# Kernel optimization log

Hardware: AMD Instinct MI355X
Metric: run time of the kernel (lower is better)

## Reference

```python
import jax, jax.numpy as jnp
import numpy as np

N = 50000      # nodes
E = 500000     # edges
MUL = 32       # multiplicity of 0e and 1o in node irreps
NUM_NEIGHBORS = 10.0
MIX = 0.15
INV3 = 1.0 / np.sqrt(3.0)  # sqrt(2*l3+1)*wigner_3j(1,1,0) = delta_ij/sqrt(3)


def setup_inputs() -> dict:
    key = jax.random.key(0)
    ks = jax.random.split(key, 16)
    f32 = jnp.float32
    node_input = jax.random.normal(ks[0], (N, 128), dtype=f32)  # 32x0e (32) + 32x1o (96)
    # edge_attr = spherical harmonics lmax=1, component normalization: Y0=1, |Y1|=sqrt(3)
    y1 = jax.random.normal(ks[1], (E, 3), dtype=f32)
    y1 = jnp.sqrt(3.0) * y1 / jnp.linalg.norm(y1, axis=1, keepdims=True)
    edge_attr = jnp.concatenate([jnp.ones((E, 1), f32), y1], axis=1)  # [E,4]
    edge_scalars = jax.random.uniform(ks[2], (E, 8), dtype=f32)       # radial embedding
    edge_src = jax.random.randint(ks[3], (E,), 0, N)
    edge_dst = jax.random.randint(ks[4], (E,), 0, N)
    rn = lambda k, s: jax.random.normal(k, s, dtype=f32)
    return {
        "node_input": node_input, "edge_attr": edge_attr, "edge_scalars": edge_scalars,
        "W1_s": rn(ks[5], (MUL, 2 * MUL)),  # first Linear, 0e block: 32 -> 64 (=feat 32 + self 32)
        "W1_v": rn(ks[6], (MUL, 2 * MUL)),  # first Linear, 1o block
        "M0": rn(ks[7], (8, 32)), "M1": rn(ks[8], (32, 32)),  # weight MLP (fc_neurons=[32,32])
        "Wtp0": rn(ks[9], (32, MUL)),   # path 0e x 0e -> 0e
        "Wtp1": rn(ks[10], (32, MUL)),  # path 0e x 1o -> 1o
        "Wtp2": rn(ks[11], (32, MUL)),  # path 1o x 0e -> 1o
        "Wtp3": rn(ks[12], (32, MUL)),  # path 1o x 1o -> 0e
        "W2_s": rn(ks[13], (2 * MUL, MUL)),  # final Linear, 0e: 64 -> 32
        "W2_v": rn(ks[14], (2 * MUL, MUL)),  # final Linear, 1o: 64 -> 32
        "edge_src": edge_src, "edge_dst": edge_dst,
    }


def _forward(node_input, edge_attr, edge_scalars, W1_s, W1_v, M0, M1,
             Wtp0, Wtp1, Wtp2, Wtp3, W2_s, W2_v, edge_src, edge_dst):
    n = node_input.shape[0]
    s = node_input[:, :MUL]                       # [N,32]  0e
    v = node_input[:, MUL:].reshape(n, MUL, 3)    # [N,32,3] 1o
    # Linear(node_input.irreps + irreps_out): per-irrep mixing, fan-in normalized
    s_all = (s @ W1_s) / jnp.sqrt(jnp.float32(MUL))                    # [N,64]
    v_all = jnp.einsum('nuk,uw->nwk', v, W1_v) / jnp.sqrt(jnp.float32(MUL))  # [N,64,3]
    feat_s, self_s = s_all[:, :MUL], s_all[:, MUL:]
    feat_v, self_v = v_all[:, :MUL], v_all[:, MUL:]

    # gather by edge source
    es = feat_s[edge_src]   # [E,32]
    ev = feat_v[edge_src]   # [E,32,3]
    y0 = edge_attr[:, 0]    # [E]
    y1 = edge_attr[:, 1:4]  # [E,3]

    # MLP on edge scalars -> per-edge, per-path 'uvu' weights (fan-in normalized)
    h = jax.nn.gelu(edge_scalars @ M0 / jnp.sqrt(jnp.float32(8)))
    h = jax.nn.gelu(h @ M1 / jnp.sqrt(jnp.float32(32)))                # [E,32]
    inv_sqrt_h = 1.0 / jnp.sqrt(jnp.float32(32))
    w0 = (h @ Wtp0) * inv_sqrt_h  # [E,32]
    w1 = (h @ Wtp1) * inv_sqrt_h
    w2 = (h @ Wtp2) * inv_sqrt_h
    w3 = (h @ Wtp3) * inv_sqrt_h

    # per-edge CG tensor product (4 'uvu' instructions)
    out0a = w0 * es * y0[:, None]                                    # 0e x 0e -> 0e
    out0b = w3 * jnp.einsum('euk,ek->eu', ev, y1) * INV3             # 1o x 1o -> 0e
    out1a = w1[:, :, None] * es[:, :, None] * y1[:, None, :]        # 0e x 1o -> 1o
    out1b = w2[:, :, None] * ev * y0[:, None, None]                 # 1o x 0e -> 1o
    out0 = jnp.concatenate([out0a, out0b], axis=1)                  # [E,64]  64x0e
    out1 = jnp.concatenate([out1a, out1b], axis=1)                  # [E,64,3] 64x1o

    # scatter-add to destination nodes, normalize by sqrt(num_neighbors)
    inv_deg = 1.0 / jnp.sqrt(jnp.float32(NUM_NEIGHBORS))
    ns = jax.ops.segment_sum(out0, edge_dst, num_segments=n) * inv_deg              # [N,64]
    nv = jax.ops.segment_sum(out1.reshape(-1, 2 * MUL * 3), edge_dst,
                             num_segments=n).reshape(n, 2 * MUL, 3) * inv_deg       # [N,64,3]

    # final per-irrep Linear to output irreps 32x0e + 32x1o
    conv_s = (ns @ W2_s) / jnp.sqrt(jnp.float32(2 * MUL))
    conv_v = jnp.einsum('nuk,uw->nwk', nv, W2_v) / jnp.sqrt(jnp.float32(2 * MUL))

    a = jnp.sqrt(jnp.float32(1.0 - MIX))
    b = jnp.sqrt(jnp.float32(MIX))
    out_s = a * self_s + b * conv_s                                  # [N,32]
    out_v = (a * self_v + b * conv_v).reshape(n, MUL * 3)            # [N,96]
    return jnp.concatenate([out_s, out_v], axis=1)                   # [N,128]


def reference(node_input, edge_attr, edge_scalars, W1_s, W1_v, M0, M1,
              Wtp0, Wtp1, Wtp2, Wtp3, W2_s, W2_v, edge_src, edge_dst):
    return _forward(node_input, edge_attr, edge_scalars, W1_s, W1_v, M0, M1,
                    Wtp0, Wtp1, Wtp2, Wtp3, W2_s, W2_v, edge_src, edge_dst)
```

## Files before the change

### kernel.cpp

```cpp
#include <hip/hip_runtime.h>
#include <math.h>

#define N_NODES 50000
#define N_EDGES 500000
#define NPB 16
#define GROUPS 8

__device__ __forceinline__ float gelu_fast(float x) {
    const float k0 = 0.7978845608028654f;
    const float k1 = 0.044715f;
    float z2 = 2.f * k0 * (x + k1 * x * x * x);
    float ez = __expf(z2);
    float th = 1.f - 2.f * __builtin_amdgcn_rcpf(ez + 1.f);
    return 0.5f * x * (1.f + th);
}

__device__ __forceinline__ unsigned short f2bf(float x) {
    unsigned int u = __float_as_uint(x);
    unsigned int r = (u + 0x7FFFu + ((u >> 16) & 1u)) >> 16;
    return (unsigned short)r;
}
__device__ __forceinline__ float bf2f(unsigned short b) {
    return __uint_as_float(((unsigned int)b) << 16);
}

__device__ __forceinline__ void lds_add(float* p, float v) {
    unsigned int off = (unsigned int)(size_t)p;
    asm volatile("ds_add_f32 %0, %1" :: "v"(off), "v"(v) : "memory");
}

__global__ void node_pre(const float* __restrict__ node_input,
                         const float* __restrict__ W1_s,
                         const float* __restrict__ W1_v,
                         float* __restrict__ feat,
                         float* __restrict__ out) {
    __shared__ float lWs[32 * 64];
    __shared__ float lWv[32 * 64];
    for (int i = threadIdx.x; i < 2048; i += blockDim.x) {
        lWs[i] = W1_s[i];
        lWv[i] = W1_v[i];
    }
    __syncthreads();
    int n = blockIdx.x * blockDim.x + threadIdx.x;
    if (n >= N_NODES) return;
    const float inv_sqrt_mul = 0.17677669529663687f;
    const float a_mix = 0.9219544457292887f;

    float s[32];
#pragma unroll
    for (int u = 0; u < 32; ++u) s[u] = node_input[n * 128 + u];
#pragma unroll 4
    for (int w = 0; w < 64; ++w) {
        float acc = 0.f;
#pragma unroll
        for (int u = 0; u < 32; ++u) acc += s[u] * lWs[u * 64 + w];
        acc *= inv_sqrt_mul;
        if (w < 32) feat[(size_t)n * 128 + w * 4 + 0] = acc;
        else        out[n * 128 + (w - 32)] = a_mix * acc;
    }
#pragma unroll
    for (int k = 0; k < 3; ++k) {
        float vk[32];
#pragma unroll
        for (int u = 0; u < 32; ++u) vk[u] = node_input[n * 128 + 32 + u * 3 + k];
#pragma unroll 4
        for (int w = 0; w < 64; ++w) {
            float acc = 0.f;
#pragma unroll
            for (int u = 0; u < 32; ++u) acc += vk[u] * lWv[u * 64 + w];
            acc *= inv_sqrt_mul;
            if (w < 32) feat[(size_t)n * 128 + w * 4 + 1 + k] = acc;
            else        out[n * 128 + 32 + (w - 32) * 3 + k] = a_mix * acc;
        }
    }
}

__global__ void hist_kernel(const int* __restrict__ edge_dst, int* __restrict__ counts) {
    int e = blockIdx.x * blockDim.x + threadIdx.x;
    if (e < N_EDGES) atomicAdd(&counts[edge_dst[e]], 1);
}

__global__ void scan_kernel(const int* __restrict__ counts,
                            int* __restrict__ offsets,
                            int* __restrict__ cursor) {
    const int T = 1024;
    __shared__ int partial[T];
    int t = threadIdx.x;
    const int chunk = (N_NODES + T - 1) / T;
    int start = t * chunk;
    int end = start + chunk; if (end > N_NODES) end = N_NODES;
    if (start > N_NODES) start = N_NODES;
    int sum = 0;
    for (int i = start; i < end; ++i) sum += counts[i];
    partial[t] = sum;
    __syncthreads();
    for (int off = 1; off < T; off <<= 1) {
        int other = (t >= off) ? partial[t - off] : 0;
        __syncthreads();
        partial[t] += other;
        __syncthreads();
    }
    int run = (t == 0) ? 0 : partial[t - 1];
    for (int i = start; i < end; ++i) {
        offsets[i] = run;
        cursor[i] = run;
        run += counts[i];
    }
    if (t == T - 1) offsets[N_NODES] = run;
}

__global__ void scatter_kernel(const int* __restrict__ edge_src,
                               const int* __restrict__ edge_dst,
                               const float* __restrict__ edge_attr,
                               const float* __restrict__ edge_scalars,
                               int* __restrict__ cursor,
                               float4* __restrict__ sS4,
                               float4* __restrict__ ySorted,
                               int2* __restrict__ srcdst) {
    int e = blockIdx.x * blockDim.x + threadIdx.x;
    if (e >= N_EDGES) return;
    int d = edge_dst[e];
    int pos = atomicAdd(&cursor[d], 1);
    float4 a  = *(const float4*)(edge_attr + (size_t)e * 4);
    float4 s0 = *(const float4*)(edge_scalars + (size_t)e * 8);
    float4 s1 = *(const float4*)(edge_scalars + (size_t)e * 8 + 4);
    ySorted[pos] = a;
    sS4[(size_t)pos * 2 + 0] = s0;
    sS4[(size_t)pos * 2 + 1] = s1;
    srcdst[pos] = make_int2(edge_src[e], d);
}

__global__ void mlp_kernel(const float4* __restrict__ sS4,
                           const float* __restrict__ M0,
                           const float* __restrict__ M1,
                           const float* __restrict__ Wtp0,
                           const float* __restrict__ Wtp1,
                           const float* __restrict__ Wtp2,
                           const float* __restrict__ Wtp3,
                           ushort4* __restrict__ wOut) {
    const int e = blockIdx.x * blockDim.x + threadIdx.x;
    if (e >= N_EDGES) return;

    const float inv_sqrt8  = 0.35355339059327373f;
    const float inv_sqrt32 = 0.17677669529663687f;

    const float4 s0 = sS4[(size_t)e * 2 + 0];
    const float4 s1 = sS4[(size_t)e * 2 + 1];

    float t[32];
#pragma unroll
    for (int u = 0; u < 32; ++u) {
        float acc = s0.x * M0[0 * 32 + u] + s0.y * M0[1 * 32 + u]
                  + s0.z * M0[2 * 32 + u] + s0.w * M0[3 * 32 + u]
                  + s1.x * M0[4 * 32 + u] + s1.y * M0[5 * 32 + u]
                  + s1.z * M0[6 * 32 + u] + s1.w * M0[7 * 32 + u];
        t[u] = gelu_fast(acc * inv_sqrt8);
    }
    float h[32];
#pragma unroll
    for (int u = 0; u < 32; ++u) {
        float acc = 0.f;
#pragma unroll
        for (int m = 0; m < 32; ++m) acc += t[m] * M1[m * 32 + u];
        h[u] = gelu_fast(acc * inv_sqrt32);
    }
    ushort4* wbase = wOut + (size_t)e * 32;
#pragma unroll 1
    for (int u = 0; u < 32; ++u) {
        float ax = 0.f, ay = 0.f, az = 0.f, aw = 0.f;
#pragma unroll
        for (int j = 0; j < 32; ++j) {
            const float hj = h[j];
            ax += hj * Wtp0[j * 32 + u];
            ay += hj * Wtp1[j * 32 + u];
            az += hj * Wtp2[j * 32 + u];
            aw += hj * Wtp3[j * 32 + u];
        }
        ushort4 o;
        o.x = f2bf(ax * inv_sqrt32);
        o.y = f2bf(ay * inv_sqrt32);
        o.z = f2bf(az * inv_sqrt32);
        o.w = f2bf(aw * inv_sqrt32);
        wbase[u] = o;
    }
}

__global__ void __launch_bounds__(256)
conv_kernel(const ushort4* __restrict__ wOut,
            const float4* __restrict__ ySorted,
            const int2* __restrict__ srcdst,
            const int* __restrict__ offsets,
            const float* __restrict__ W2_s,
            const float* __restrict__ W2_v,
            const float* __restrict__ feat,
            float* __restrict__ out) {
    __shared__ float sacc[NPB * 256];
    for (int i = threadIdx.x; i < NPB * 256; i += blockDim.x) sacc[i] = 0.f;
    __syncthreads();

    const int lane = threadIdx.x & 31;
    const int g = threadIdx.x >> 5;
    const int n0 = blockIdx.x * NPB;
    const int eb = offsets[n0];
    const int ee = offsets[n0 + NPB];
    const float INV3 = 0.5773502691896258f;
    const float4* feat4 = (const float4*)feat;

    const int total = ee - eb;
    const int per = (total + GROUPS - 1) / GROUPS;
    const int es = eb + g * per;
    int et = es + per; if (et > ee) et = ee;

    float r0 = 0.f, r1 = 0.f, r2 = 0.f, r3 = 0.f;
    float r4 = 0.f, r5 = 0.f, r6 = 0.f, r7 = 0.f;
    int cur = -1;

#pragma unroll 2
    for (int e = es; e < et; ++e) {
        const int2 sd = srcdst[e];
        const ushort4 wq = wOut[(size_t)e * 32 + lane];
        const float4 yq = ySorted[e];
        const float4 f = feat4[(size_t)sd.x * 32 + lane];

        if (sd.y != cur) {
            if (cur >= 0) {
                float* a = sacc + (cur - n0) * 256;
                lds_add(a + lane, r0);
                lds_add(a + 32 + lane, r1);
                lds_add(a + 64 + lane * 3 + 0, r2);
                lds_add(a + 64 + lane * 3 + 1, r3);
                lds_add(a + 64 + lane * 3 + 2, r4);
                lds_add(a + 160 + lane * 3 + 0, r5);
                lds_add(a + 160 + lane * 3 + 1, r6);
                lds_add(a + 160 + lane * 3 + 2, r7);
            }
            cur = sd.y;
            r0 = r1 = r2 = r3 = r4 = r5 = r6 = r7 = 0.f;
        }

        const float w0 = bf2f(wq.x), w1 = bf2f(wq.y);
        const float w2 = bf2f(wq.z), w3 = bf2f(wq.w);
        const float dvy = f.y * yq.y + f.z * yq.z + f.w * yq.w;
        const float w1es = w1 * f.x;
        const float w2y0 = w2 * yq.x;

        r0 += w0 * f.x * yq.x;
        r1 += w3 * dvy * INV3;
        r2 += w1es * yq.y;
        r3 += w1es * yq.z;
        r4 += w1es * yq.w;
        r5 += w2y0 * f.y;
        r6 += w2y0 * f.z;
        r7 += w2y0 * f.w;
    }
    if (cur >= 0) {
        float* a = sacc + (cur - n0) * 256;
        lds_add(a + lane, r0);
        lds_add(a + 32 + lane, r1);
        lds_add(a + 64 + lane * 3 + 0, r2);
        lds_add(a + 64 + lane * 3 + 1, r3);
        lds_add(a + 64 + lane * 3 + 2, r4);
        lds_add(a + 160 + lane * 3 + 0, r5);
        lds_add(a + 160 + lane * 3 + 1, r6);
        lds_add(a + 160 + lane * 3 + 2, r7);
    }
    asm volatile("s_waitcnt lgkmcnt(0)" ::: "memory");
    __syncthreads();

    const float scale = 0.31622776601683794f * 0.125f * 0.3872983346207417f;
    for (int li = g; li < NPB; li += GROUPS) {
        const float* a = sacc + li * 256;
        float cs = 0.f, cv0 = 0.f, cv1 = 0.f, cv2 = 0.f;
#pragma unroll 8
        for (int j = 0; j < 64; ++j) {
            const float as = a[j];
            cs += as * __ldg(&W2_s[j * 32 + lane]);
            const float wv = __ldg(&W2_v[j * 32 + lane]);
            cv0 += a[64 + 3 * j + 0] * wv;
            cv1 += a[64 + 3 * j + 1] * wv;
            cv2 += a[64 + 3 * j + 2] * wv;
        }
        float* o = out + (size_t)(n0 + li) * 128;
        o[lane]              += scale * cs;
        o[32 + lane * 3 + 0] += scale * cv0;
        o[32 + lane * 3 + 1] += scale * cv1;
        o[32 + lane * 3 + 2] += scale * cv2;
    }
}

extern "C" void kernel_launch(void* const* d_in, const int* in_sizes, int n_in,
                              void* d_out, int out_size, void* d_ws, size_t ws_size,
                              hipStream_t stream) {
    const float* node_input   = (const float*)d_in[0];
    const float* edge_attr    = (const float*)d_in[1];
    const float* edge_scalars = (const float*)d_in[2];
    const float* W1_s = (const float*)d_in[3];
    const float* W1_v = (const float*)d_in[4];
    const float* M0   = (const float*)d_in[5];
    const float* M1   = (const float*)d_in[6];
    const float* Wtp0 = (const float*)d_in[7];
    const float* Wtp1 = (const float*)d_in[8];
    const float* Wtp2 = (const float*)d_in[9];
    const float* Wtp3 = (const float*)d_in[10];
    const float* W2_s = (const float*)d_in[11];
    const float* W2_v = (const float*)d_in[12];
    const int* edge_src = (const int*)d_in[13];
    const int* edge_dst = (const int*)d_in[14];
    float* out = (float*)d_out;
    float* ws  = (float*)d_ws;

    float*  feat    = ws;
    float4* sS4     = (float4*)(feat + (size_t)N_NODES * 128);
    float4* ySorted = sS4 + (size_t)N_EDGES * 2;
    ushort4* wOut   = (ushort4*)(ySorted + N_EDGES);
    int2*  srcdst   = (int2*)(wOut + (size_t)N_EDGES * 32);
    int*   counts   = (int*)(srcdst + N_EDGES);
    int*   offsets  = counts + N_NODES;
    int*   cursor   = offsets + N_NODES + 1;

    hipMemsetAsync(counts, 0, N_NODES * sizeof(int), stream);

    node_pre<<<(N_NODES + 255) / 256, 256, 0, stream>>>(node_input, W1_s, W1_v,
                                                        feat, out);

    hist_kernel<<<(N_EDGES + 255) / 256, 256, 0, stream>>>(edge_dst, counts);
    scan_kernel<<<1, 1024, 0, stream>>>(counts, offsets, cursor);
    scatter_kernel<<<(N_EDGES + 255) / 256, 256, 0, stream>>>(edge_src, edge_dst,
                                                              edge_attr, edge_scalars,
                                                              cursor, sS4, ySorted, srcdst);

    mlp_kernel<<<(N_EDGES + 255) / 256, 256, 0, stream>>>(sS4, M0, M1,
                                                          Wtp0, Wtp1, Wtp2, Wtp3, wOut);

    conv_kernel<<<N_NODES / NPB, 256, 0, stream>>>(wOut, ySorted, srcdst, offsets,
                                                   W2_s, W2_v, feat, out);
}
```

Before: 587.8 us.

## Run edge MLP in original edge order and coalesce its weight writes via LDS

The scatter kernel no longer permutes edge_scalars. It stores an int4 (src, dst, original edge id) per sorted position, and the MLP reads edge_scalars directly in original order. The MLP now stages its bf16 per-edge weights in shared memory and writes them out coalesced instead of as strided per-thread stores. In exchange, the conv kernel gathers wOut through the original edge index, which makes that large read a random 256-byte row gather instead of a sequential stream, and the index record grows from 8 to 16 bytes.

```diff
diff --git a/kernel.cpp b/kernel.cpp
--- a/kernel.cpp
+++ b/kernel.cpp
@@ -112,25 +112,18 @@
 __global__ void scatter_kernel(const int* __restrict__ edge_src,
                                const int* __restrict__ edge_dst,
                                const float* __restrict__ edge_attr,
-                               const float* __restrict__ edge_scalars,
                                int* __restrict__ cursor,
-                               float4* __restrict__ sS4,
                                float4* __restrict__ ySorted,
-                               int2* __restrict__ srcdst) {
+                               int4* __restrict__ sde) {
     int e = blockIdx.x * blockDim.x + threadIdx.x;
     if (e >= N_EDGES) return;
     int d = edge_dst[e];
     int pos = atomicAdd(&cursor[d], 1);
-    float4 a  = *(const float4*)(edge_attr + (size_t)e * 4);
-    float4 s0 = *(const float4*)(edge_scalars + (size_t)e * 8);
-    float4 s1 = *(const float4*)(edge_scalars + (size_t)e * 8 + 4);
-    ySorted[pos] = a;
-    sS4[(size_t)pos * 2 + 0] = s0;
-    sS4[(size_t)pos * 2 + 1] = s1;
-    srcdst[pos] = make_int2(edge_src[e], d);
-}
-
-__global__ void mlp_kernel(const float4* __restrict__ sS4,
+    ySorted[pos] = *(const float4*)(edge_attr + (size_t)e * 4);
+    sde[pos] = make_int4(edge_src[e], d, e, 0);
+}
+
+__global__ void mlp_kernel(const float* __restrict__ edge_scalars,
                            const float* __restrict__ M0,
                            const float* __restrict__ M1,
                            const float* __restrict__ Wtp0,
@@ -138,14 +131,17 @@
                            const float* __restrict__ Wtp2,
                            const float* __restrict__ Wtp3,
                            ushort4* __restrict__ wOut) {
-    const int e = blockIdx.x * blockDim.x + threadIdx.x;
-    if (e >= N_EDGES) return;
+    __shared__ ushort4 stage[256][17];
+
+    const int e0 = blockIdx.x * 256;
+    int e = e0 + threadIdx.x;
+    int ec = e < N_EDGES ? e : N_EDGES - 1;
 
     const float inv_sqrt8  = 0.35355339059327373f;
     const float inv_sqrt32 = 0.17677669529663687f;
 
-    const float4 s0 = sS4[(size_t)e * 2 + 0];
-    const float4 s1 = sS4[(size_t)e * 2 + 1];
+    const float4 s0 = *(const float4*)(edge_scalars + (size_t)ec * 8);
+    const float4 s1 = *(const float4*)(edge_scalars + (size_t)ec * 8 + 4);
 
     float t[32];
 #pragma unroll
@@ -164,31 +160,45 @@
         for (int m = 0; m < 32; ++m) acc += t[m] * M1[m * 32 + u];
         h[u] = gelu_fast(acc * inv_sqrt32);
     }
-    ushort4* wbase = wOut + (size_t)e * 32;
 #pragma unroll 1
-    for (int u = 0; u < 32; ++u) {
-        float ax = 0.f, ay = 0.f, az = 0.f, aw = 0.f;
-#pragma unroll
-        for (int j = 0; j < 32; ++j) {
-            const float hj = h[j];
-            ax += hj * Wtp0[j * 32 + u];
-            ay += hj * Wtp1[j * 32 + u];
-            az += hj * Wtp2[j * 32 + u];
-            aw += hj * Wtp3[j * 32 + u];
-        }
-        ushort4 o;
-        o.x = f2bf(ax * inv_sqrt32);
-        o.y = f2bf(ay * inv_sqrt32);
-        o.z = f2bf(az * inv_sqrt32);
-        o.w = f2bf(aw * inv_sqrt32);
-        wbase[u] = o;
+    for (int half = 0; half < 2; ++half) {
+#pragma unroll 1
+        for (int u1 = 0; u1 < 16; ++u1) {
+            const int u = half * 16 + u1;
+            float ax = 0.f, ay = 0.f, az = 0.f, aw = 0.f;
+#pragma unroll
+            for (int j = 0; j < 32; ++j) {
+                const float hj = h[j];
+                ax += hj * Wtp0[j * 32 + u];
+                ay += hj * Wtp1[j * 32 + u];
+                az += hj * Wtp2[j * 32 + u];
+                aw += hj * Wtp3[j * 32 + u];
+            }
+            ushort4 o;
+            o.x = f2bf(ax * inv_sqrt32);
+            o.y = f2bf(ay * inv_sqrt32);
+            o.z = f2bf(az * inv_sqrt32);
+            o.w = f2bf(aw * inv_sqrt32);
+            stage[threadIdx.x][u1] = o;
+        }
+        __syncthreads();
+#pragma unroll
+        for (int p = 0; p < 16; ++p) {
+            const int k = p * 256 + threadIdx.x;
+            const int el = k >> 4;
+            const int u1 = k & 15;
+            const int ge = e0 + el;
+            if (ge < N_EDGES)
+                wOut[(size_t)ge * 32 + half * 16 + u1] = stage[el][u1];
+        }
+        __syncthreads();
     }
 }
 
 __global__ void __launch_bounds__(256)
 conv_kernel(const ushort4* __restrict__ wOut,
             const float4* __restrict__ ySorted,
-            const int2* __restrict__ srcdst,
+            const int4* __restrict__ sde,
             const int* __restrict__ offsets,
             const float* __restrict__ W2_s,
             const float* __restrict__ W2_v,
@@ -217,8 +227,8 @@
 
 #pragma unroll 2
     for (int e = es; e < et; ++e) {
-        const int2 sd = srcdst[e];
-        const ushort4 wq = wOut[(size_t)e * 32 + lane];
+        const int4 sd = sde[e];
+        const ushort4 wq = wOut[(size_t)sd.z * 32 + lane];
         const float4 yq = ySorted[e];
         const float4 f = feat4[(size_t)sd.x * 32 + lane];
 
@@ -310,11 +320,10 @@
     float* ws  = (float*)d_ws;
 
     float*  feat    = ws;
-    float4* sS4     = (float4*)(feat + (size_t)N_NODES * 128);
-    float4* ySorted = sS4 + (size_t)N_EDGES * 2;
+    float4* ySorted = (float4*)(feat + (size_t)N_NODES * 128);
     ushort4* wOut   = (ushort4*)(ySorted + N_EDGES);
-    int2*  srcdst   = (int2*)(wOut + (size_t)N_EDGES * 32);
-    int*   counts   = (int*)(srcdst + N_EDGES);
+    int4*  sde      = (int4*)(wOut + (size_t)N_EDGES * 32);
+    int*   counts   = (int*)(sde + N_EDGES);
     int*   offsets  = counts + N_NODES;
     int*   cursor   = offsets + N_NODES + 1;
 
@@ -326,12 +335,12 @@
     hist_kernel<<<(N_EDGES + 255) / 256, 256, 0, stream>>>(edge_dst, counts);
     scan_kernel<<<1, 1024, 0, stream>>>(counts, offsets, cursor);
     scatter_kernel<<<(N_EDGES + 255) / 256, 256, 0, stream>>>(edge_src, edge_dst,
-                                                              edge_attr, edge_scalars,
-                                                              cursor, sS4, ySorted, srcdst);
-
-    mlp_kernel<<<(N_EDGES + 255) / 256, 256, 0, stream>>>(sS4, M0, M1,
+                                                              edge_attr,
+                                                              cursor, ySorted, sde);
+
+    mlp_kernel<<<(N_EDGES + 255) / 256, 256, 0, stream>>>(edge_scalars, M0, M1,
                                                           Wtp0, Wtp1, Wtp2, Wtp3, wOut);
 
-    conv_kernel<<<N_NODES / NPB, 256, 0, stream>>>(wOut, ySorted, srcdst, offsets,
+    conv_kernel<<<N_NODES / NPB, 256, 0, stream>>>(wOut, ySorted, sde, offsets,
                                                    W2_s, W2_v, feat, out);
 }
```

Result: faster. 574.3 us (-2.3%).
